# Optimization experiments

Measured on AMD Instinct MI355X. Metric: run time of the kernel, lower is better.

Reference implementation:

```python
import jax, jax.numpy as jnp
import numpy as np

N_NODES = 100000
IN_DIM = 128
HIDDEN = 256
N_CLASSES = 16
N_EDGES = 1600000
N_GRAPHS = 64


def setup_inputs() -> dict:
    key = jax.random.key(0)
    ks = jax.random.split(key, 12)
    x = jax.random.normal(ks[0], (N_NODES, IN_DIM), dtype=jnp.float32)
    edge_index = jax.random.randint(ks[1], (2, N_EDGES), 0, N_NODES, dtype=jnp.int64)
    batch = jnp.sort(jax.random.randint(ks[2], (N_NODES,), 0, N_GRAPHS, dtype=jnp.int64))
    s = 0.05
    # SAGEConv layer 1: lin_l (on aggregated neighbors, with bias), lin_r (on root, no bias)
    W1l = jax.random.normal(ks[3], (IN_DIM, HIDDEN), dtype=jnp.float32) * s
    b1 = jnp.zeros((HIDDEN,), dtype=jnp.float32)
    W1r = jax.random.normal(ks[4], (IN_DIM, HIDDEN), dtype=jnp.float32) * s
    # SAGEConv layer 2
    W2l = jax.random.normal(ks[5], (HIDDEN, HIDDEN), dtype=jnp.float32) * s
    b2 = jnp.zeros((HIDDEN,), dtype=jnp.float32)
    W2r = jax.random.normal(ks[6], (HIDDEN, HIDDEN), dtype=jnp.float32) * s
    # final classifier
    fcW = jax.random.normal(ks[7], (HIDDEN, N_CLASSES), dtype=jnp.float32) * s
    fcb = jnp.zeros((N_CLASSES,), dtype=jnp.float32)
    return {"x": x, "edge_index": edge_index, "batch": batch,
            "W1l": W1l, "b1": b1, "W1r": W1r,
            "W2l": W2l, "b2": b2, "W2r": W2r,
            "fcW": fcW, "fcb": fcb}


def _sage_conv(x, src, dst, Wl, bl, Wr, n_nodes):
    # mean aggregation of neighbor features onto destination nodes
    agg = jax.ops.segment_sum(x[src], dst, num_segments=n_nodes)      # [N, d]
    deg = jax.ops.segment_sum(jnp.ones(src.shape, x.dtype), dst, num_segments=n_nodes)
    mean = agg / jnp.maximum(deg, 1.0)[:, None]
    # out = lin_l(mean_neighbors) + lin_r(x_root)  (PyG SAGEConv, mean aggr)
    return mean @ Wl + bl + x @ Wr


def reference(x, edge_index, batch, W1l, b1, W1r, W2l, b2, W2r, fcW, fcb):
    src, dst = edge_index[0], edge_index[1]
    h = jax.nn.relu(_sage_conv(x, src, dst, W1l, b1, W1r, N_NODES))
    # dropout is identity in inference mode
    h = jax.nn.relu(_sage_conv(h, src, dst, W2l, b2, W2r, N_NODES))
    # global mean pool over graphs in the batch
    g_sum = jax.ops.segment_sum(h, batch, num_segments=N_GRAPHS)      # [G, d]
    g_cnt = jax.ops.segment_sum(jnp.ones(batch.shape, h.dtype), batch, num_segments=N_GRAPHS)
    g = g_sum / jnp.maximum(g_cnt, 1.0)[:, None]
    return g @ fcW + fcb                                              # [G, num_classes]
```

## Files before the change

kernel.cpp:

```cpp
#include <hip/hip_runtime.h>

#define INDIM 128
#define HID 256
#define NCLS 16
#define NGRAPH 64
#define CHUNK 8192

typedef __bf16 bf16_t;
typedef bf16_t bf16x8 __attribute__((ext_vector_type(8)));
typedef float f32x4 __attribute__((ext_vector_type(4)));

__device__ __forceinline__ float bfu_lo(unsigned v) {
    union { unsigned i; float f; } u; u.i = v << 16; return u.f;
}
__device__ __forceinline__ float bfu_hi(unsigned v) {
    union { unsigned i; float f; } u; u.i = v & 0xffff0000u; return u.f;
}
__device__ __forceinline__ unsigned short f2bf(float f) {
    union { float f; unsigned i; } u; u.f = f;
    unsigned b = u.i;
    return (unsigned short)((b + 0x7fffu + ((b >> 16) & 1u)) >> 16);
}
__device__ __forceinline__ unsigned packbf(float lo, float hi) {
    return (unsigned)f2bf(lo) | ((unsigned)f2bf(hi) << 16);
}

typedef __attribute__((address_space(1))) const unsigned gu32_t;
typedef __attribute__((address_space(3))) unsigned lu32_t;
__device__ __forceinline__ void gl_lds16(const void* g, void* l) {
    __builtin_amdgcn_global_load_lds((gu32_t*)g, (lu32_t*)l, 16, 0, 0);
}

#define ACC8(a, v)                                   \
    do {                                             \
        a[0] += bfu_lo((v).x); a[1] += bfu_hi((v).x); \
        a[2] += bfu_lo((v).y); a[3] += bfu_hi((v).y); \
        a[4] += bfu_lo((v).z); a[5] += bfu_hi((v).z); \
        a[6] += bfu_lo((v).w); a[7] += bfu_hi((v).w); \
    } while (0)

__global__ void hist_kernel(const int* __restrict__ dst, int* __restrict__ deg, int E) {
    int e = blockIdx.x * blockDim.x + threadIdx.x;
    if (e < E) atomicAdd(&deg[dst[e]], 1);
}

__global__ void scan1_kernel(const int* __restrict__ deg, int* __restrict__ bsum, int n) {
    __shared__ int s[256];
    int t = threadIdx.x;
    int i = blockIdx.x * 256 + t;
    s[t] = (i < n) ? deg[i] : 0;
    __syncthreads();
    for (int off = 128; off > 0; off >>= 1) {
        if (t < off) s[t] += s[t + off];
        __syncthreads();
    }
    if (t == 0) bsum[blockIdx.x] = s[0];
}

__global__ void scan2_kernel(int* bsum, int nb) {
    __shared__ int s[1024];
    int t = threadIdx.x;
    int v = (t < nb) ? bsum[t] : 0;
    s[t] = v;
    __syncthreads();
    for (int off = 1; off < 1024; off <<= 1) {
        int u = (t >= off) ? s[t - off] : 0;
        __syncthreads();
        s[t] += u;
        __syncthreads();
    }
    if (t < nb) bsum[t] = s[t] - v;
}

__global__ void scan3_kernel(const int* __restrict__ deg, const int* __restrict__ bsum,
                             int* __restrict__ offs, int* __restrict__ gcur, int n) {
    __shared__ int s[256];
    int t = threadIdx.x;
    int i = blockIdx.x * 256 + t;
    int v = (i < n) ? deg[i] : 0;
    s[t] = v;
    __syncthreads();
    for (int off = 1; off < 256; off <<= 1) {
        int u = (t >= off) ? s[t - off] : 0;
        __syncthreads();
        s[t] += u;
        __syncthreads();
    }
    if (i < n) offs[i] = s[t] - v + bsum[blockIdx.x];
    if (t == 0) gcur[blockIdx.x] = bsum[blockIdx.x];
}

__global__ __launch_bounds__(256) void binA_kernel(const int* __restrict__ src,
                                                   const int* __restrict__ dst,
                                                   int* __restrict__ gcur,
                                                   unsigned* __restrict__ tmp,
                                                   int E, int nbuck) {
    __shared__ int hist[512];
    __shared__ int base[512];
    int t = threadIdx.x;
    int e0 = blockIdx.x * CHUNK;
    int e1 = min(e0 + CHUNK, E);
    for (int i = t; i < nbuck; i += 256) hist[i] = 0;
    __syncthreads();
    for (int e = e0 + t; e < e1; e += 256) atomicAdd(&hist[dst[e] >> 8], 1);
    __syncthreads();
    for (int i = t; i < nbuck; i += 256) {
        int c = hist[i];
        base[i] = (c > 0) ? atomicAdd(&gcur[i], c) : 0;
    }
    __syncthreads();
    for (int e = e0 + t; e < e1; e += 256) {
        int d = dst[e];
        int p = atomicAdd(&base[d >> 8], 1);
        tmp[p] = ((unsigned)(d & 255) << 17) | (unsigned)src[e];
    }
}

__global__ __launch_bounds__(256) void binB_kernel(const unsigned* __restrict__ tmp,
                                                   const int* __restrict__ offs,
                                                   int* __restrict__ srclist, int E, int n) {
    __shared__ int cur[256];
    int b = blockIdx.x;
    int node0 = b << 8;
    int nnodes = min(256, n - node0);
    int t = threadIdx.x;
    if (t < nnodes) cur[t] = offs[node0 + t];
    __syncthreads();
    int ebeg = offs[node0];
    int eend = (node0 + 256 < n) ? offs[node0 + 256] : E;
    for (int e = ebeg + t; e < eend; e += 256) {
        unsigned v = tmp[e];
        int p = atomicAdd(&cur[v >> 17], 1);
        srclist[p] = (int)(v & 0x1FFFFu);
    }
}

__global__ void prep_kernel(const float* __restrict__ x, unsigned short* __restrict__ xb,
                            const float* __restrict__ W1l, const float* __restrict__ W1r,
                            unsigned short* __restrict__ Bt1,
                            const float* __restrict__ W2l, const float* __restrict__ W2r,
                            unsigned short* __restrict__ Bt2, int castb) {
    int b = blockIdx.x, t = threadIdx.x;
    if (b < castb) {
        int i4 = (b * 256 + t) * 4;
        float4 v = *(const float4*)(x + i4);
        *(ushort4*)(xb + i4) = make_ushort4(f2bf(v.x), f2bf(v.y), f2bf(v.z), f2bf(v.w));
    } else if (b < castb + 256) {
        int idx = (b - castb) * 256 + t;
        int nn = idx >> 8, k = idx & 255;
        float v = (k < 128) ? W1l[(size_t)k * 256 + nn] : W1r[(size_t)(k - 128) * 256 + nn];
        Bt1[(size_t)nn * 256 + k] = f2bf(v);
    } else {
        int idx = (b - castb - 256) * 256 + t;
        int nn = idx >> 9, k = idx & 511;
        float v = (k < 256) ? W2l[(size_t)k * 256 + nn] : W2r[(size_t)(k - 256) * 256 + nn];
        Bt2[(size_t)nn * 512 + k] = f2bf(v);
    }
}

__global__ void agg1_kernel(const unsigned short* __restrict__ xb, const int* __restrict__ srclist,
                            const int* __restrict__ offs, const int* __restrict__ deg,
                            unsigned short* __restrict__ mean, int n) {
    int gid = blockIdx.x * blockDim.x + threadIdx.x;
    int node = gid >> 6, lane = gid & 63;
    if (node >= n) return;
    int q = lane >> 4, sub = lane & 15;
    int st = __builtin_amdgcn_readfirstlane(offs[node]);
    int d = __builtin_amdgcn_readfirstlane(deg[node]);
    int end = st + d;
    float aA[8] = {0, 0, 0, 0, 0, 0, 0, 0}, aB[8] = {0, 0, 0, 0, 0, 0, 0, 0};
    const unsigned short* rb = xb + sub * 8;
    int e = st;
    for (; e + 7 < end; e += 8) {
        int s0 = srclist[e + q];
        int s1 = srclist[e + 4 + q];
        uint4 v0 = *(const uint4*)(rb + (size_t)s0 * 128);
        uint4 v1 = *(const uint4*)(rb + (size_t)s1 * 128);
        ACC8(aA, v0);
        ACC8(aB, v1);
    }
    for (; e + 3 < end; e += 4) {
        int s0 = srclist[e + q];
        uint4 v0 = *(const uint4*)(rb + (size_t)s0 * 128);
        ACC8(aA, v0);
    }
    int rem = end - e;
    if (rem > 0) {
        int s0 = srclist[e + ((q < rem) ? q : 0)];
        uint4 v0 = *(const uint4*)(rb + (size_t)s0 * 128);
        if (q < rem) ACC8(aA, v0);
    }
    float inv = 1.f / fmaxf((float)d, 1.f);
    float tot[8];
#pragma unroll
    for (int i = 0; i < 8; ++i) {
        float s = aA[i] + aB[i];
        s += __shfl_xor(s, 16);
        s += __shfl_xor(s, 32);
        tot[i] = s * inv;
    }
    if (lane < 16) {
        uint4 o;
        o.x = packbf(tot[0], tot[1]);
        o.y = packbf(tot[2], tot[3]);
        o.z = packbf(tot[4], tot[5]);
        o.w = packbf(tot[6], tot[7]);
        *(uint4*)(mean + (size_t)node * 128 + sub * 8) = o;
    }
}

__global__ void agg2_kernel(const unsigned short* __restrict__ h1, const int* __restrict__ srclist,
                            const int* __restrict__ offs, const int* __restrict__ deg,
                            unsigned short* __restrict__ mean, int n) {
    int gid = blockIdx.x * blockDim.x + threadIdx.x;
    int node = gid >> 6, lane = gid & 63;
    if (node >= n) return;
    int half = lane >> 5, sub = lane & 31;
    int st = __builtin_amdgcn_readfirstlane(offs[node]);
    int d = __builtin_amdgcn_readfirstlane(deg[node]);
    int end = st + d;
    float aA[8] = {0, 0, 0, 0, 0, 0, 0, 0}, aB[8] = {0, 0, 0, 0, 0, 0, 0, 0};
    float aC[8] = {0, 0, 0, 0, 0, 0, 0, 0}, aD[8] = {0, 0, 0, 0, 0, 0, 0, 0};
    const unsigned short* rb = h1 + sub * 8;
    int e = st;
    for (; e + 7 < end; e += 8) {
        int s0 = srclist[e + half];
        int s1 = srclist[e + 2 + half];
        int s2 = srclist[e + 4 + half];
        int s3 = srclist[e + 6 + half];
        uint4 v0 = *(const uint4*)(rb + (size_t)s0 * 256);
        uint4 v1 = *(const uint4*)(rb + (size_t)s1 * 256);
        uint4 v2 = *(const uint4*)(rb + (size_t)s2 * 256);
        uint4 v3 = *(const uint4*)(rb + (size_t)s3 * 256);
        ACC8(aA, v0);
        ACC8(aB, v1);
        ACC8(aC, v2);
        ACC8(aD, v3);
    }
    for (; e + 1 < end; e += 2) {
        int s0 = srclist[e + half];
        uint4 v0 = *(const uint4*)(rb + (size_t)s0 * 256);
        ACC8(aA, v0);
    }
    if (e < end) {
        int s0 = srclist[e];
        uint4 v0 = *(const uint4*)(rb + (size_t)s0 * 256);
        if (half == 0) ACC8(aA, v0);
    }
    float inv = 1.f / fmaxf((float)d, 1.f);
    float tot[8];
#pragma unroll
    for (int i = 0; i < 8; ++i) {
        float s = (aA[i] + aB[i]) + (aC[i] + aD[i]);
        s += __shfl_xor(s, 32);
        tot[i] = s * inv;
    }
    if (half == 0) {
        uint4 o;
        o.x = packbf(tot[0], tot[1]);
        o.y = packbf(tot[2], tot[3]);
        o.z = packbf(tot[4], tot[5]);
        o.w = packbf(tot[6], tot[7]);
        *(uint4*)(mean + (size_t)node * 256 + sub * 8) = o;
    }
}

template <int KH>
__global__ __launch_bounds__(256) void gemm_kernel(
        const bf16_t* __restrict__ A1, const bf16_t* __restrict__ A2,
        const bf16_t* __restrict__ Bt, const float* __restrict__ bias,
        unsigned short* __restrict__ H, int M) {
    constexpr int KT = 2 * KH;
    constexpr int NC = KT / 64;
    constexpr int CPH = KH / 64;
    __shared__ unsigned short As[64 * 64];
    int t = threadIdx.x, wave = t >> 6, lane = t & 63;
    int quad = lane >> 4, l16 = lane & 15;
    int row0 = blockIdx.x * 64, n0 = wave * 64;

    f32x4 acc[4][4];
#pragma unroll
    for (int i = 0; i < 4; ++i)
#pragma unroll
        for (int j = 0; j < 4; ++j) acc[i][j] = (f32x4)(0.f);

    int rA = wave * 8 + (lane >> 3);
    int kb = lane & 7;
    int kswA = (kb ^ (rA & 7)) << 3;
    unsigned short* ldsA = &As[(size_t)(wave * 8) * 64];
    unsigned short* ldsB = &As[(size_t)(32 + wave * 8) * 64];

    const bf16_t* Bp = Bt + (size_t)(n0 + l16) * KT + quad * 8;

    for (int c = 0; c < NC; ++c) {
        const bf16_t* Ah = (c < CPH) ? A1 : A2;
        int kk = ((c < CPH) ? c : (c - CPH)) * 64;
        gl_lds16(Ah + (size_t)(row0 + rA) * KH + kk + kswA, ldsA);
        gl_lds16(Ah + (size_t)(row0 + 32 + rA) * KH + kk + kswA, ldsB);
        __syncthreads();
        int bk = c * 64;
#pragma unroll
        for (int sub = 0; sub < 2; ++sub) {
            bf16x8 af[4], bfr[4];
#pragma unroll
            for (int mi = 0; mi < 4; ++mi) {
                int r = mi * 16 + l16;
                int qb = sub * 4 + quad;
                af[mi] = *(const bf16x8*)&As[r * 64 + ((qb ^ (r & 7)) << 3)];
            }
#pragma unroll
            for (int ni = 0; ni < 4; ++ni)
                bfr[ni] = *(const bf16x8*)(Bp + (size_t)(ni * 16) * KT + bk + sub * 32);
#pragma unroll
            for (int mi = 0; mi < 4; ++mi)
#pragma unroll
                for (int ni = 0; ni < 4; ++ni)
                    acc[mi][ni] = __builtin_amdgcn_mfma_f32_16x16x32_bf16(
                        af[mi], bfr[ni], acc[mi][ni], 0, 0, 0);
        }
        __syncthreads();
    }

    float bv[4];
#pragma unroll
    for (int ni = 0; ni < 4; ++ni) bv[ni] = bias[n0 + ni * 16 + l16];
#pragma unroll
    for (int mi = 0; mi < 4; ++mi) {
#pragma unroll
        for (int r = 0; r < 4; ++r) {
            int row = row0 + mi * 16 + quad * 4 + r;
            if (row < M) {
#pragma unroll
                for (int ni = 0; ni < 4; ++ni) {
                    int col = n0 + ni * 16 + l16;
                    H[(size_t)row * 256 + col] = f2bf(fmaxf(acc[mi][ni][r] + bv[ni], 0.f));
                }
            }
        }
    }
}

__global__ __launch_bounds__(256) void pool_kernel(const unsigned short* __restrict__ h2,
                                                   const int* __restrict__ batch,
                                                   float* __restrict__ g, float* __restrict__ cnt,
                                                   int n) {
    int col = threadIdx.x;
    int row0 = blockIdx.x * 64;
    int rend = min(row0 + 64, n);
    float acc = 0.f;
    int cur = -1, seglen = 0;
    int r = row0;
    for (; r + 3 < rend; r += 4) {
        int b0 = batch[r], b1 = batch[r + 1], b2 = batch[r + 2], b3 = batch[r + 3];
        unsigned short v0 = h2[(size_t)r * 256 + col];
        unsigned short v1 = h2[(size_t)(r + 1) * 256 + col];
        unsigned short v2 = h2[(size_t)(r + 2) * 256 + col];
        unsigned short v3 = h2[(size_t)(r + 3) * 256 + col];
        int bs[4] = {b0, b1, b2, b3};
        unsigned short vs[4] = {v0, v1, v2, v3};
#pragma unroll
        for (int j = 0; j < 4; ++j) {
            if (bs[j] != cur) {
                if (cur >= 0) {
                    atomicAdd(&g[cur * 256 + col], acc);
                    if (col == 0) atomicAdd(&cnt[cur], (float)seglen);
                }
                acc = 0.f; cur = bs[j]; seglen = 0;
            }
            union { unsigned i; float f; } u;
            u.i = ((unsigned)vs[j]) << 16;
            acc += u.f;
            seglen++;
        }
    }
    for (; r < rend; ++r) {
        int b = batch[r];
        if (b != cur) {
            if (cur >= 0) {
                atomicAdd(&g[cur * 256 + col], acc);
                if (col == 0) atomicAdd(&cnt[cur], (float)seglen);
            }
            acc = 0.f; cur = b; seglen = 0;
        }
        union { unsigned i; float f; } u;
        u.i = ((unsigned)h2[(size_t)r * 256 + col]) << 16;
        acc += u.f;
        seglen++;
    }
    if (cur >= 0) {
        atomicAdd(&g[cur * 256 + col], acc);
        if (col == 0) atomicAdd(&cnt[cur], (float)seglen);
    }
}

__global__ void final_kernel(const float* __restrict__ g, const float* __restrict__ cnt,
                             const float* __restrict__ fcW, const float* __restrict__ fcb,
                             float* __restrict__ out) {
    int t = threadIdx.x;
    for (int o = t; o < NGRAPH * NCLS; o += 256) {
        int gi = o >> 4, c = o & 15;
        float inv = 1.f / fmaxf(cnt[gi], 1.f);
        float dot = 0.f;
        for (int k = 0; k < 256; ++k) dot += g[gi * 256 + k] * fcW[k * 16 + c];
        out[o] = dot * inv + fcb[c];
    }
}

extern "C" void kernel_launch(void* const* d_in, const int* in_sizes, int n_in, void* d_out,
                              int out_size, void* d_ws, size_t ws_size, hipStream_t stream) {
    const float* x   = (const float*)d_in[0];
    const int* edge  = (const int*)d_in[1];
    const int* batch = (const int*)d_in[2];
    const float* W1l = (const float*)d_in[3];
    const float* b1  = (const float*)d_in[4];
    const float* W1r = (const float*)d_in[5];
    const float* W2l = (const float*)d_in[6];
    const float* b2  = (const float*)d_in[7];
    const float* W2r = (const float*)d_in[8];
    const float* fcW = (const float*)d_in[9];
    const float* fcb = (const float*)d_in[10];
    float* out = (float*)d_out;

    const int n = in_sizes[0] / INDIM;
    const int E = in_sizes[1] / 2;
    const int* src = edge;
    const int* dst = edge + E;
    const int nbuck = (n + 255) >> 8;

    char* ws = (char*)d_ws;
    size_t off = 0;
    auto alloc = [&](size_t bytes) {
        size_t p = off;
        off = (off + bytes + 511) & ~(size_t)511;
        return p;
    };
    size_t offs_o    = alloc((size_t)n * 4);
    size_t deg_o     = alloc((size_t)n * 4);
    size_t cnt_o     = alloc(64 * 4);
    size_t g_o       = alloc(64 * 256 * 4);
    size_t zero_end  = off;
    size_t bsum_o    = alloc(1024 * 4);
    size_t gcur_o    = alloc(512 * 4);
    size_t srclist_o = alloc((size_t)E * 4);
    size_t bt1_o     = alloc(256 * 256 * 2);
    size_t bt2_o     = alloc(256 * 512 * 2);
    size_t xbm2_o    = alloc((size_t)n * 256 * 2);
    size_t mean1_o   = alloc((size_t)n * 128 * 2);
    size_t h1_o      = alloc((size_t)n * 256 * 2);
    size_t h2_o      = alloc((size_t)n * 256 * 2);

    int*   offs    = (int*)(ws + offs_o);
    int*   deg     = (int*)(ws + deg_o);
    float* cnt     = (float*)(ws + cnt_o);
    float* g       = (float*)(ws + g_o);
    int*   bsum    = (int*)(ws + bsum_o);
    int*   gcur    = (int*)(ws + gcur_o);
    int*   srclist = (int*)(ws + srclist_o);
    unsigned short* Bt1   = (unsigned short*)(ws + bt1_o);
    unsigned short* Bt2   = (unsigned short*)(ws + bt2_o);
    unsigned short* xb16  = (unsigned short*)(ws + xbm2_o);
    unsigned short* mean2 = (unsigned short*)(ws + xbm2_o);
    unsigned short* mean1 = (unsigned short*)(ws + mean1_o);
    unsigned short* h1b   = (unsigned short*)(ws + h1_o);
    unsigned*       tmp   = (unsigned*)(ws + h2_o);
    unsigned short* h2b   = (unsigned short*)(ws + h2_o);

    hipMemsetAsync(ws + deg_o, 0, zero_end - deg_o, stream);

    int eb = (E + 255) / 256;
    int nb = (n + 255) / 256;
    hist_kernel<<<eb, 256, 0, stream>>>(dst, deg, E);
    scan1_kernel<<<nb, 256, 0, stream>>>(deg, bsum, n);
    scan2_kernel<<<1, 1024, 0, stream>>>(bsum, nb);
    scan3_kernel<<<nb, 256, 0, stream>>>(deg, bsum, offs, gcur, n);
    binA_kernel<<<(E + CHUNK - 1) / CHUNK, 256, 0, stream>>>(src, dst, gcur, tmp, E, nbuck);
    binB_kernel<<<nbuck, 256, 0, stream>>>(tmp, offs, srclist, E, n);

    int castb = n * INDIM / 4 / 256;
    prep_kernel<<<castb + 256 + 512, 256, 0, stream>>>(x, xb16, W1l, W1r, Bt1, W2l, W2r, Bt2, castb);

    int aggb = (n * 64 + 255) / 256;
    int gemmb = (n + 63) / 64;

    agg1_kernel<<<aggb, 256, 0, stream>>>(xb16, srclist, offs, deg, mean1, n);
    gemm_kernel<128><<<gemmb, 256, 0, stream>>>(
        (const bf16_t*)mean1, (const bf16_t*)xb16, (const bf16_t*)Bt1, b1, h1b, n);
    agg2_kernel<<<aggb, 256, 0, stream>>>(h1b, srclist, offs, deg, mean2, n);
    gemm_kernel<256><<<gemmb, 256, 0, stream>>>(
        (const bf16_t*)mean2, (const bf16_t*)h1b, (const bf16_t*)Bt2, b2, h2b, n);

    pool_kernel<<<(n + 63) / 64, 256, 0, stream>>>(h2b, batch, g, cnt, n);
    final_kernel<<<1, 256, 0, stream>>>(g, cnt, fcW, fcb, out);
}
```

Before: 572.2 us.

## Quantize gathered node features to int8 with global scale for neighbor aggregation

Computes a global abs-max of x (in prep) and of h1 (in the GEMM epilogue via atomicMax), quantizes the features to offset int8 in new kernels, and makes both aggregation kernels gather int8 rows. Accumulation uses packed 16-bit integer lanes, and the result is dequantized at the end. This halves the bytes gathered per edge in the bandwidth-bound scatter-mean phase. In exchange it adds two quantization passes and coarse per-tensor 8-bit precision. The packed 16-bit lane sums overflow only past roughly 256 neighbours, so very high-degree nodes would give wrong results.

```diff
diff --git a/kernel.cpp b/kernel.cpp
--- a/kernel.cpp
+++ b/kernel.cpp
@@ -31,12 +31,16 @@
     __builtin_amdgcn_global_load_lds((gu32_t*)g, (lu32_t*)l, 16, 0, 0);
 }
 
-#define ACC8(a, v)                                   \
+#define IACC(aE, aO, v)                              \
     do {                                             \
-        a[0] += bfu_lo((v).x); a[1] += bfu_hi((v).x); \
-        a[2] += bfu_lo((v).y); a[3] += bfu_hi((v).y); \
-        a[4] += bfu_lo((v).z); a[5] += bfu_hi((v).z); \
-        a[6] += bfu_lo((v).w); a[7] += bfu_hi((v).w); \
+        aE[0] += ((v).x & 0x00FF00FFu);              \
+        aO[0] += (((v).x >> 8) & 0x00FF00FFu);       \
+        aE[1] += ((v).y & 0x00FF00FFu);              \
+        aO[1] += (((v).y >> 8) & 0x00FF00FFu);       \
+        aE[2] += ((v).z & 0x00FF00FFu);              \
+        aO[2] += (((v).z >> 8) & 0x00FF00FFu);       \
+        aE[3] += ((v).w & 0x00FF00FFu);              \
+        aO[3] += (((v).w >> 8) & 0x00FF00FFu);       \
     } while (0)
 
 __global__ void hist_kernel(const int* __restrict__ dst, int* __restrict__ deg, int E) {
@@ -139,12 +143,17 @@
                             const float* __restrict__ W1l, const float* __restrict__ W1r,
                             unsigned short* __restrict__ Bt1,
                             const float* __restrict__ W2l, const float* __restrict__ W2r,
-                            unsigned short* __restrict__ Bt2, int castb) {
+                            unsigned short* __restrict__ Bt2, unsigned* __restrict__ gmaxx,
+                            int castb) {
     int b = blockIdx.x, t = threadIdx.x;
     if (b < castb) {
         int i4 = (b * 256 + t) * 4;
         float4 v = *(const float4*)(x + i4);
         *(ushort4*)(xb + i4) = make_ushort4(f2bf(v.x), f2bf(v.y), f2bf(v.z), f2bf(v.w));
+        float m = fmaxf(fmaxf(fabsf(v.x), fabsf(v.y)), fmaxf(fabsf(v.z), fabsf(v.w)));
+#pragma unroll
+        for (int off = 32; off > 0; off >>= 1) m = fmaxf(m, __shfl_xor(m, off));
+        if ((t & 63) == 0) atomicMax(gmaxx, __float_as_uint(m));
     } else if (b < castb + 256) {
         int idx = (b - castb) * 256 + t;
         int nn = idx >> 8, k = idx & 255;
@@ -158,110 +167,157 @@
     }
 }
 
-__global__ void agg1_kernel(const unsigned short* __restrict__ xb, const int* __restrict__ srclist,
+__global__ void quantx_kernel(const float* __restrict__ x, const float* __restrict__ gmaxp,
+                              unsigned* __restrict__ xq, int total4) {
+    int idx = blockIdx.x * blockDim.x + threadIdx.x;
+    if (idx >= total4) return;
+    float inv = 127.f / fmaxf(*gmaxp, 1e-20f);
+    float4 v = *(const float4*)(x + idx * 4);
+    int b0 = (int)fminf(fmaxf(rintf(v.x * inv), -127.f), 127.f) + 128;
+    int b1 = (int)fminf(fmaxf(rintf(v.y * inv), -127.f), 127.f) + 128;
+    int b2 = (int)fminf(fmaxf(rintf(v.z * inv), -127.f), 127.f) + 128;
+    int b3 = (int)fminf(fmaxf(rintf(v.w * inv), -127.f), 127.f) + 128;
+    xq[idx] = (unsigned)b0 | ((unsigned)b1 << 8) | ((unsigned)b2 << 16) | ((unsigned)b3 << 24);
+}
+
+__global__ void quanth_kernel(const unsigned short* __restrict__ h1, const float* __restrict__ gmaxp,
+                              unsigned* __restrict__ hq, int total4) {
+    int idx = blockIdx.x * blockDim.x + threadIdx.x;
+    if (idx >= total4) return;
+    float inv = 127.f / fmaxf(*gmaxp, 1e-20f);
+    uint2 v = *(const uint2*)(h1 + idx * 4);
+    int b0 = (int)fminf(rintf(bfu_lo(v.x) * inv), 127.f) + 128;
+    int b1 = (int)fminf(rintf(bfu_hi(v.x) * inv), 127.f) + 128;
+    int b2 = (int)fminf(rintf(bfu_lo(v.y) * inv), 127.f) + 128;
+    int b3 = (int)fminf(rintf(bfu_hi(v.y) * inv), 127.f) + 128;
+    hq[idx] = (unsigned)b0 | ((unsigned)b1 << 8) | ((unsigned)b2 << 16) | ((unsigned)b3 << 24);
+}
+
+__global__ void agg1_kernel(const unsigned char* __restrict__ xq, const int* __restrict__ srclist,
                             const int* __restrict__ offs, const int* __restrict__ deg,
+                            const float* __restrict__ gmaxp,
                             unsigned short* __restrict__ mean, int n) {
     int gid = blockIdx.x * blockDim.x + threadIdx.x;
     int node = gid >> 6, lane = gid & 63;
     if (node >= n) return;
-    int q = lane >> 4, sub = lane & 15;
+    int g = lane >> 3, sub = lane & 7;
     int st = __builtin_amdgcn_readfirstlane(offs[node]);
     int d = __builtin_amdgcn_readfirstlane(deg[node]);
     int end = st + d;
-    float aA[8] = {0, 0, 0, 0, 0, 0, 0, 0}, aB[8] = {0, 0, 0, 0, 0, 0, 0, 0};
-    const unsigned short* rb = xb + sub * 8;
+    unsigned aE[4] = {0, 0, 0, 0}, aO[4] = {0, 0, 0, 0};
+    unsigned bE[4] = {0, 0, 0, 0}, bO[4] = {0, 0, 0, 0};
+    const unsigned char* rb = xq + sub * 16;
     int e = st;
-    for (; e + 7 < end; e += 8) {
-        int s0 = srclist[e + q];
-        int s1 = srclist[e + 4 + q];
+    for (; e + 15 < end; e += 16) {
+        int s0 = srclist[e + g];
+        int s1 = srclist[e + 8 + g];
         uint4 v0 = *(const uint4*)(rb + (size_t)s0 * 128);
         uint4 v1 = *(const uint4*)(rb + (size_t)s1 * 128);
-        ACC8(aA, v0);
-        ACC8(aB, v1);
-    }
-    for (; e + 3 < end; e += 4) {
-        int s0 = srclist[e + q];
+        IACC(aE, aO, v0);
+        IACC(bE, bO, v1);
+    }
+    for (; e + 7 < end; e += 8) {
+        int s0 = srclist[e + g];
         uint4 v0 = *(const uint4*)(rb + (size_t)s0 * 128);
-        ACC8(aA, v0);
+        IACC(aE, aO, v0);
     }
     int rem = end - e;
     if (rem > 0) {
-        int s0 = srclist[e + ((q < rem) ? q : 0)];
+        int s0 = srclist[e + ((g < rem) ? g : 0)];
         uint4 v0 = *(const uint4*)(rb + (size_t)s0 * 128);
-        if (q < rem) ACC8(aA, v0);
-    }
-    float inv = 1.f / fmaxf((float)d, 1.f);
-    float tot[8];
-#pragma unroll
-    for (int i = 0; i < 8; ++i) {
-        float s = aA[i] + aB[i];
-        s += __shfl_xor(s, 16);
-        s += __shfl_xor(s, 32);
-        tot[i] = s * inv;
-    }
-    if (lane < 16) {
-        uint4 o;
-        o.x = packbf(tot[0], tot[1]);
-        o.y = packbf(tot[2], tot[3]);
-        o.z = packbf(tot[4], tot[5]);
-        o.w = packbf(tot[6], tot[7]);
-        *(uint4*)(mean + (size_t)node * 128 + sub * 8) = o;
-    }
-}
-
-__global__ void agg2_kernel(const unsigned short* __restrict__ h1, const int* __restrict__ srclist,
+        if (g < rem) IACC(aE, aO, v0);
+    }
+#pragma unroll
+    for (int j = 0; j < 4; ++j) {
+        unsigned se = aE[j] + bE[j], so = aO[j] + bO[j];
+        se += (unsigned)__shfl_xor((int)se, 8);
+        se += (unsigned)__shfl_xor((int)se, 16);
+        se += (unsigned)__shfl_xor((int)se, 32);
+        so += (unsigned)__shfl_xor((int)so, 8);
+        so += (unsigned)__shfl_xor((int)so, 16);
+        so += (unsigned)__shfl_xor((int)so, 32);
+        aE[j] = se;
+        aO[j] = so;
+    }
+    if (g == 0) {
+        float sc = (*gmaxp) * (1.f / 127.f);
+        float invd = 1.f / fmaxf((float)d, 1.f);
+        unsigned o[8];
+#pragma unroll
+        for (int j = 0; j < 4; ++j) {
+            float m0 = sc * (float)((int)(aE[j] & 0xFFFFu) - 128 * d) * invd;
+            float m1 = sc * (float)((int)(aO[j] & 0xFFFFu) - 128 * d) * invd;
+            float m2 = sc * (float)((int)(aE[j] >> 16) - 128 * d) * invd;
+            float m3 = sc * (float)((int)(aO[j] >> 16) - 128 * d) * invd;
+            o[j * 2] = packbf(m0, m1);
+            o[j * 2 + 1] = packbf(m2, m3);
+        }
+        uint4* p = (uint4*)(mean + (size_t)node * 128 + sub * 16);
+        p[0] = make_uint4(o[0], o[1], o[2], o[3]);
+        p[1] = make_uint4(o[4], o[5], o[6], o[7]);
+    }
+}
+
+__global__ void agg2_kernel(const unsigned char* __restrict__ hq, const int* __restrict__ srclist,
                             const int* __restrict__ offs, const int* __restrict__ deg,
+                            const float* __restrict__ gmaxp,
                             unsigned short* __restrict__ mean, int n) {
     int gid = blockIdx.x * blockDim.x + threadIdx.x;
     int node = gid >> 6, lane = gid & 63;
     if (node >= n) return;
-    int half = lane >> 5, sub = lane & 31;
+    int g = lane >> 4, sub = lane & 15;
     int st = __builtin_amdgcn_readfirstlane(offs[node]);
     int d = __builtin_amdgcn_readfirstlane(deg[node]);
     int end = st + d;
-    float aA[8] = {0, 0, 0, 0, 0, 0, 0, 0}, aB[8] = {0, 0, 0, 0, 0, 0, 0, 0};
-    float aC[8] = {0, 0, 0, 0, 0, 0, 0, 0}, aD[8] = {0, 0, 0, 0, 0, 0, 0, 0};
-    const unsigned short* rb = h1 + sub * 8;
+    unsigned aE[4] = {0, 0, 0, 0}, aO[4] = {0, 0, 0, 0};
+    unsigned bE[4] = {0, 0, 0, 0}, bO[4] = {0, 0, 0, 0};
+    const unsigned char* rb = hq + sub * 16;
     int e = st;
     for (; e + 7 < end; e += 8) {
-        int s0 = srclist[e + half];
-        int s1 = srclist[e + 2 + half];
-        int s2 = srclist[e + 4 + half];
-        int s3 = srclist[e + 6 + half];
+        int s0 = srclist[e + g];
+        int s1 = srclist[e + 4 + g];
         uint4 v0 = *(const uint4*)(rb + (size_t)s0 * 256);
         uint4 v1 = *(const uint4*)(rb + (size_t)s1 * 256);
-        uint4 v2 = *(const uint4*)(rb + (size_t)s2 * 256);
-        uint4 v3 = *(const uint4*)(rb + (size_t)s3 * 256);
-        ACC8(aA, v0);
-        ACC8(aB, v1);
-        ACC8(aC, v2);
-        ACC8(aD, v3);
-    }
-    for (; e + 1 < end; e += 2) {
-        int s0 = srclist[e + half];
+        IACC(aE, aO, v0);
+        IACC(bE, bO, v1);
+    }
+    for (; e + 3 < end; e += 4) {
+        int s0 = srclist[e + g];
         uint4 v0 = *(const uint4*)(rb + (size_t)s0 * 256);
-        ACC8(aA, v0);
-    }
-    if (e < end) {
-        int s0 = srclist[e];
+        IACC(aE, aO, v0);
+    }
+    int rem = end - e;
+    if (rem > 0) {
+        int s0 = srclist[e + ((g < rem) ? g : 0)];
         uint4 v0 = *(const uint4*)(rb + (size_t)s0 * 256);
-        if (half == 0) ACC8(aA, v0);
-    }
-    float inv = 1.f / fmaxf((float)d, 1.f);
-    float tot[8];
-#pragma unroll
-    for (int i = 0; i < 8; ++i) {
-        float s = (aA[i] + aB[i]) + (aC[i] + aD[i]);
-        s += __shfl_xor(s, 32);
-        tot[i] = s * inv;
-    }
-    if (half == 0) {
-        uint4 o;
-        o.x = packbf(tot[0], tot[1]);
-        o.y = packbf(tot[2], tot[3]);
-        o.z = packbf(tot[4], tot[5]);
-        o.w = packbf(tot[6], tot[7]);
-        *(uint4*)(mean + (size_t)node * 256 + sub * 8) = o;
+        if (g < rem) IACC(aE, aO, v0);
+    }
+#pragma unroll
+    for (int j = 0; j < 4; ++j) {
+        unsigned se = aE[j] + bE[j], so = aO[j] + bO[j];
+        se += (unsigned)__shfl_xor((int)se, 16);
+        se += (unsigned)__shfl_xor((int)se, 32);
+        so += (unsigned)__shfl_xor((int)so, 16);
+        so += (unsigned)__shfl_xor((int)so, 32);
+        aE[j] = se;
+        aO[j] = so;
+    }
+    if (g == 0) {
+        float sc = (*gmaxp) * (1.f / 127.f);
+        float invd = 1.f / fmaxf((float)d, 1.f);
+        unsigned o[8];
+#pragma unroll
+        for (int j = 0; j < 4; ++j) {
+            float m0 = sc * (float)((int)(aE[j] & 0xFFFFu) - 128 * d) * invd;
+            float m1 = sc * (float)((int)(aO[j] & 0xFFFFu) - 128 * d) * invd;
+            float m2 = sc * (float)((int)(aE[j] >> 16) - 128 * d) * invd;
+            float m3 = sc * (float)((int)(aO[j] >> 16) - 128 * d) * invd;
+            o[j * 2] = packbf(m0, m1);
+            o[j * 2 + 1] = packbf(m2, m3);
+        }
+        uint4* p = (uint4*)(mean + (size_t)node * 256 + sub * 16);
+        p[0] = make_uint4(o[0], o[1], o[2], o[3]);
+        p[1] = make_uint4(o[4], o[5], o[6], o[7]);
     }
 }
 
@@ -269,7 +325,7 @@
 __global__ __launch_bounds__(256) void gemm_kernel(
         const bf16_t* __restrict__ A1, const bf16_t* __restrict__ A2,
         const bf16_t* __restrict__ Bt, const float* __restrict__ bias,
-        unsigned short* __restrict__ H, int M) {
+        unsigned short* __restrict__ H, unsigned* __restrict__ gmaxout, int M) {
     constexpr int KT = 2 * KH;
     constexpr int NC = KT / 64;
     constexpr int CPH = KH / 64;
@@ -324,6 +380,7 @@
     float bv[4];
 #pragma unroll
     for (int ni = 0; ni < 4; ++ni) bv[ni] = bias[n0 + ni * 16 + l16];
+    float mloc = 0.f;
 #pragma unroll
     for (int mi = 0; mi < 4; ++mi) {
 #pragma unroll
@@ -333,10 +390,17 @@
 #pragma unroll
                 for (int ni = 0; ni < 4; ++ni) {
                     int col = n0 + ni * 16 + l16;
-                    H[(size_t)row * 256 + col] = f2bf(fmaxf(acc[mi][ni][r] + bv[ni], 0.f));
+                    float hv = fmaxf(acc[mi][ni][r] + bv[ni], 0.f);
+                    mloc = fmaxf(mloc, hv);
+                    H[(size_t)row * 256 + col] = f2bf(hv);
                 }
             }
         }
+    }
+    if (gmaxout) {
+#pragma unroll
+        for (int off = 32; off > 0; off >>= 1) mloc = fmaxf(mloc, __shfl_xor(mloc, off));
+        if (lane == 0) atomicMax(gmaxout, __float_as_uint(mloc));
     }
 }
 
@@ -438,6 +502,7 @@
     size_t deg_o     = alloc((size_t)n * 4);
     size_t cnt_o     = alloc(64 * 4);
     size_t g_o       = alloc(64 * 256 * 4);
+    size_t gmax_o    = alloc(8);
     size_t zero_end  = off;
     size_t bsum_o    = alloc(1024 * 4);
     size_t gcur_o    = alloc(512 * 4);
@@ -453,16 +518,20 @@
     int*   deg     = (int*)(ws + deg_o);
     float* cnt     = (float*)(ws + cnt_o);
     float* g       = (float*)(ws + g_o);
+    unsigned* gmaxx = (unsigned*)(ws + gmax_o);
+    unsigned* gmaxh = (unsigned*)(ws + gmax_o + 4);
     int*   bsum    = (int*)(ws + bsum_o);
     int*   gcur    = (int*)(ws + gcur_o);
     int*   srclist = (int*)(ws + srclist_o);
     unsigned short* Bt1   = (unsigned short*)(ws + bt1_o);
     unsigned short* Bt2   = (unsigned short*)(ws + bt2_o);
     unsigned short* xb16  = (unsigned short*)(ws + xbm2_o);
+    unsigned char*  xq8   = (unsigned char*)(ws + xbm2_o + (size_t)n * 256);
     unsigned short* mean2 = (unsigned short*)(ws + xbm2_o);
     unsigned short* mean1 = (unsigned short*)(ws + mean1_o);
     unsigned short* h1b   = (unsigned short*)(ws + h1_o);
     unsigned*       tmp   = (unsigned*)(ws + h2_o);
+    unsigned char*  hq8   = (unsigned char*)(ws + h2_o + (size_t)n * 256);
     unsigned short* h2b   = (unsigned short*)(ws + h2_o);
 
     hipMemsetAsync(ws + deg_o, 0, zero_end - deg_o, stream);
@@ -477,17 +546,23 @@
     binB_kernel<<<nbuck, 256, 0, stream>>>(tmp, offs, srclist, E, n);
 
     int castb = n * INDIM / 4 / 256;
-    prep_kernel<<<castb + 256 + 512, 256, 0, stream>>>(x, xb16, W1l, W1r, Bt1, W2l, W2r, Bt2, castb);
+    prep_kernel<<<castb + 256 + 512, 256, 0, stream>>>(x, xb16, W1l, W1r, Bt1, W2l, W2r, Bt2,
+                                                       gmaxx, castb);
+    int xq4 = n * INDIM / 4;
+    quantx_kernel<<<(xq4 + 255) / 256, 256, 0, stream>>>(x, (const float*)gmaxx, (unsigned*)xq8, xq4);
 
     int aggb = (n * 64 + 255) / 256;
     int gemmb = (n + 63) / 64;
 
-    agg1_kernel<<<aggb, 256, 0, stream>>>(xb16, srclist, offs, deg, mean1, n);
+    agg1_kernel<<<aggb, 256, 0, stream>>>(xq8, srclist, offs, deg, (const float*)gmaxx, mean1, n);
     gemm_kernel<128><<<gemmb, 256, 0, stream>>>(
-        (const bf16_t*)mean1, (const bf16_t*)xb16, (const bf16_t*)Bt1, b1, h1b, n);
-    agg2_kernel<<<aggb, 256, 0, stream>>>(h1b, srclist, offs, deg, mean2, n);
+        (const bf16_t*)mean1, (const bf16_t*)xb16, (const bf16_t*)Bt1, b1, h1b, gmaxh, n);
+    int hq4 = n * HID / 4;
+    quanth_kernel<<<(hq4 + 255) / 256, 256, 0, stream>>>(h1b, (const float*)gmaxh, (unsigned*)hq8, hq4);
+    agg2_kernel<<<aggb, 256, 0, stream>>>(hq8, srclist, offs, deg, (const float*)gmaxh, mean2, n);
     gemm_kernel<256><<<gemmb, 256, 0, stream>>>(
-        (const bf16_t*)mean2, (const bf16_t*)h1b, (const bf16_t*)Bt2, b2, h2b, n);
+        (const bf16_t*)mean2, (const bf16_t*)h1b, (const bf16_t*)Bt2, b2, h2b,
+        (unsigned*)nullptr, n);
 
     pool_kernel<<<(n + 63) / 64, 256, 0, stream>>>(h2b, batch, g, cnt, n);
     final_kernel<<<1, 256, 0, stream>>>(g, cnt, fcW, fcb, out);
```

Result: slower. 1.152 ms (+101.4%).
